# Kernel optimization log

Hardware: AMD Instinct MI355X
Metric: run time of the kernel (lower is better)

## Reference

```python
import jax, jax.numpy as jnp
import numpy as np


def setup_inputs() -> dict:
    key = jax.random.key(0)
    ks = jax.random.split(key, 7)
    B, C, N, D = 32, 256, 4096, 256
    s = 0.05
    return {
        "x": jax.random.normal(ks[0], (B, C, N), dtype=jnp.float32),
        "Wq": jax.random.normal(ks[1], (D, C), dtype=jnp.float32) * s,
        "bq": jax.random.normal(ks[2], (D,), dtype=jnp.float32) * s,
        "Wk": jax.random.normal(ks[3], (D, C), dtype=jnp.float32) * s,
        "bk": jax.random.normal(ks[4], (D,), dtype=jnp.float32) * s,
        "Wv": jax.random.normal(ks[5], (D, C), dtype=jnp.float32) * s,
        "bv": jax.random.normal(ks[6], (D,), dtype=jnp.float32) * s,
    }


def reference(x, Wq, bq, Wk, bk, Wv, bv):
    # 1x1 Conv1d == per-timestep linear: [B,C,N] x [D,C] -> [B,D,N]
    Q = jnp.einsum("bcn,dc->bdn", x, Wq) + bq[None, :, None]
    K = jnp.einsum("bcn,dc->bdn", x, Wk) + bk[None, :, None]
    V = jnp.einsum("bcn,dc->bdn", x, Wv) + bv[None, :, None]
    N = x.shape[-1]
    scale = 1.0 / jnp.sqrt(jnp.asarray(N, dtype=x.dtype))
    # channel-attention: scores are [B, D, D] (Q @ K^T over the time axis)
    scores = jnp.einsum("bdn,ben->bde", Q, K) * scale
    weights = jax.nn.softmax(scores, axis=-1)
    out = jnp.einsum("bde,ben->bdn", weights, V)  # [B, D, N]
    return out
```

## Files before the change

kernel.cpp:

```cpp
#include <hip/hip_runtime.h>
#include <cstdint>
#include <cstddef>


typedef float f32x4 __attribute__((ext_vector_type(4)));
typedef __bf16 bf16x8 __attribute__((ext_vector_type(8)));
typedef unsigned short u16;
typedef u16 u16x8 __attribute__((ext_vector_type(8)));
typedef u16 u16x4 __attribute__((ext_vector_type(4)));

__device__ __forceinline__ u16 f2bf(float f) {
    unsigned u = __builtin_bit_cast(unsigned, f);
    u += 0x7FFFu + ((u >> 16) & 1u);
    return (u16)(u >> 16);
}

__device__ __forceinline__ f32x4 mfma16(bf16x8 a, bf16x8 b, f32x4 c) {
    return __builtin_amdgcn_mfma_f32_16x16x32_bf16(a, b, c, 0, 0, 0);
}

__global__ void k_wvt(const float* __restrict__ Wv, u16* __restrict__ WvT) {
    const int eb = blockIdx.x;
    const int c  = threadIdx.x;
    u16x8 pk;
#pragma unroll
    for (int j = 0; j < 8; ++j) pk[j] = f2bf(Wv[(eb * 8 + j) * 256 + c]);
    *(u16x8*)&WvT[c * 256 + eb * 8] = pk;
}

__global__ void k_wcvt(const float* __restrict__ Wq, const float* __restrict__ Wk,
                       u16* __restrict__ Wqb, u16* __restrict__ Wkb) {
    const int m = blockIdx.x >> 5, chunk = blockIdx.x & 31;
    const float* src = m == 0 ? Wq : Wk;
    u16* dst = m == 0 ? Wqb : Wkb;
    const int i = chunk * 2048 + threadIdx.x * 8;
    f32x4 w0 = *(const f32x4*)(src + i);
    f32x4 w1 = *(const f32x4*)(src + i + 4);
    u16x8 pk;
    pk[0] = f2bf(w0[0]); pk[1] = f2bf(w0[1]); pk[2] = f2bf(w0[2]); pk[3] = f2bf(w0[3]);
    pk[4] = f2bf(w1[0]); pk[5] = f2bf(w1[1]); pk[6] = f2bf(w1[2]); pk[7] = f2bf(w1[3]);
    *(u16x8*)&dst[i] = pk;
}

__global__ __launch_bounds__(512, 2) void k_gram_p(const float* __restrict__ x,
                                                   float* __restrict__ Gpart,
                                                   float* __restrict__ rsum) {
    __shared__ __align__(16) u16 lds[2][256 * 64];
    __shared__ float ldsr[256];
    const int b = blockIdx.x >> 3, split = blockIdx.x & 7;
    const int t = threadIdx.x;
    const int lane = t & 63, wid = t >> 6;
    const int g = lane >> 4, q = lane & 15;

    if (t < 256) ldsr[t] = 0.f;

    f32x4 zero4 = {0.f, 0.f, 0.f, 0.f};
    f32x4 acc[2][16];
#pragma unroll
    for (int i = 0; i < 2; ++i)
#pragma unroll
        for (int j = 0; j < 16; ++j) acc[i][j] = zero4;

    const int c_st = t >> 1, half = t & 1;
    const int swz_w = (c_st & 7) << 3;
    const float* xp = x + ((size_t)b * 256 + c_st) * 4096 + split * 512 + half * 32;

    float s = 0.f;
    f32x4 R[8];
#pragma unroll
    for (int j = 0; j < 8; ++j) R[j] = *(const f32x4*)(xp + j * 4);
#pragma unroll
    for (int kk = 0; kk < 4; ++kk) {
        f32x4 w0 = R[2 * kk], w1 = R[2 * kk + 1];
        s += w0[0] + w0[1] + w0[2] + w0[3] + w1[0] + w1[1] + w1[2] + w1[3];
        u16x8 pk;
        pk[0] = f2bf(w0[0]); pk[1] = f2bf(w0[1]); pk[2] = f2bf(w0[2]); pk[3] = f2bf(w0[3]);
        pk[4] = f2bf(w1[0]); pk[5] = f2bf(w1[1]); pk[6] = f2bf(w1[2]); pk[7] = f2bf(w1[3]);
        *(u16x8*)&lds[0][(c_st * 64 + half * 32 + kk * 8) ^ swz_w] = pk;
    }
    __syncthreads();

    for (int nc = 0; nc < 8; ++nc) {
        const int cur = nc & 1;
        if (nc < 7) {
#pragma unroll
            for (int j = 0; j < 8; ++j) R[j] = *(const f32x4*)(xp + (nc + 1) * 64 + j * 4);
        }
#pragma unroll
        for (int ks = 0; ks < 2; ++ks) {
            const int c0 = 32 * wid + q;
            const int c1 = c0 + 16;
            bf16x8 a0 = *(const bf16x8*)&lds[cur][(c0 * 64 + ks * 32 + g * 8) ^ ((c0 & 7) << 3)];
            bf16x8 a1 = *(const bf16x8*)&lds[cur][(c1 * 64 + ks * 32 + g * 8) ^ ((c1 & 7) << 3)];
#pragma unroll
            for (int et = 0; et < 16; ++et) {
                const int c2 = et * 16 + q;
                bf16x8 bb = *(const bf16x8*)&lds[cur][(c2 * 64 + ks * 32 + g * 8) ^ ((c2 & 7) << 3)];
                acc[0][et] = mfma16(a0, bb, acc[0][et]);
                acc[1][et] = mfma16(a1, bb, acc[1][et]);
            }
        }
        if (nc < 7) {
#pragma unroll
            for (int kk = 0; kk < 4; ++kk) {
                f32x4 w0 = R[2 * kk], w1 = R[2 * kk + 1];
                s += w0[0] + w0[1] + w0[2] + w0[3] + w1[0] + w1[1] + w1[2] + w1[3];
                u16x8 pk;
                pk[0] = f2bf(w0[0]); pk[1] = f2bf(w0[1]); pk[2] = f2bf(w0[2]); pk[3] = f2bf(w0[3]);
                pk[4] = f2bf(w1[0]); pk[5] = f2bf(w1[1]); pk[6] = f2bf(w1[2]); pk[7] = f2bf(w1[3]);
                *(u16x8*)&lds[cur ^ 1][(c_st * 64 + half * 32 + kk * 8) ^ swz_w] = pk;
            }
        }
        __syncthreads();
    }

    atomicAdd(&ldsr[c_st], s);

    float* gp = Gpart + (size_t)(split * 32 + b) * 65536;
#pragma unroll
    for (int dt = 0; dt < 2; ++dt)
#pragma unroll
        for (int et = 0; et < 16; ++et)
#pragma unroll
            for (int rr = 0; rr < 4; ++rr) {
                const int cc = 32 * wid + dt * 16 + 4 * g + rr;
                const int c2 = et * 16 + q;
                gp[cc * 256 + c2] = acc[dt][et][rr];
            }
    __syncthreads();
    if (t < 256) atomicAdd(&rsum[b * 256 + t], ldsr[t]);
}

__global__ void k_reduce(const float* __restrict__ Gpart, u16* __restrict__ Gb) {
    const size_t j = (size_t)blockIdx.x * 2048 + threadIdx.x * 8;
    f32x4 s0 = {0.f, 0.f, 0.f, 0.f}, s1 = {0.f, 0.f, 0.f, 0.f};
#pragma unroll
    for (int s = 0; s < 8; ++s) {
        s0 += *(const f32x4*)(Gpart + (size_t)s * 2097152 + j);
        s1 += *(const f32x4*)(Gpart + (size_t)s * 2097152 + j + 4);
    }
    u16x8 pk;
    pk[0] = f2bf(s0[0]); pk[1] = f2bf(s0[1]); pk[2] = f2bf(s0[2]); pk[3] = f2bf(s0[3]);
    pk[4] = f2bf(s1[0]); pk[5] = f2bf(s1[1]); pk[6] = f2bf(s1[2]); pk[7] = f2bf(s1[3]);
    *(u16x8*)&Gb[j] = pk;
}

__global__ __launch_bounds__(512, 2) void k_gram(const float* __restrict__ x,
                                                 float* __restrict__ G,
                                                 float* __restrict__ rsum) {
    __shared__ __align__(16) u16 lds[256 * 64];
    __shared__ float ldsr[256];
    const int b = blockIdx.x >> 3, split = blockIdx.x & 7;
    const int t = threadIdx.x;
    const int lane = t & 63, wid = t >> 6;
    const int g = lane >> 4, q = lane & 15;

    if (t < 256) ldsr[t] = 0.f;

    f32x4 zero4 = {0.f, 0.f, 0.f, 0.f};
    f32x4 acc[2][16];
#pragma unroll
    for (int i = 0; i < 2; ++i)
#pragma unroll
        for (int j = 0; j < 16; ++j) acc[i][j] = zero4;

    const int c_st = t >> 1, half = t & 1;
    const int swz_w = (c_st & 7) << 3;
    const float* xp = x + ((size_t)b * 256 + c_st) * 4096 + split * 512 + half * 32;

    for (int nc = 0; nc < 8; ++nc) {
        __syncthreads();
        float s = 0.f;
#pragma unroll
        for (int kk = 0; kk < 4; ++kk) {
            f32x4 w0 = *(const f32x4*)(xp + nc * 64 + kk * 8);
            f32x4 w1 = *(const f32x4*)(xp + nc * 64 + kk * 8 + 4);
            s += w0[0] + w0[1] + w0[2] + w0[3] + w1[0] + w1[1] + w1[2] + w1[3];
            u16x8 pk;
            pk[0] = f2bf(w0[0]); pk[1] = f2bf(w0[1]); pk[2] = f2bf(w0[2]); pk[3] = f2bf(w0[3]);
            pk[4] = f2bf(w1[0]); pk[5] = f2bf(w1[1]); pk[6] = f2bf(w1[2]); pk[7] = f2bf(w1[3]);
            *(u16x8*)&lds[(c_st * 64 + half * 32 + kk * 8) ^ swz_w] = pk;
        }
        atomicAdd(&ldsr[c_st], s);
        __syncthreads();
#pragma unroll
        for (int ks = 0; ks < 2; ++ks) {
            const int c0 = 32 * wid + q;
            const int c1 = c0 + 16;
            bf16x8 a0 = *(const bf16x8*)&lds[(c0 * 64 + ks * 32 + g * 8) ^ ((c0 & 7) << 3)];
            bf16x8 a1 = *(const bf16x8*)&lds[(c1 * 64 + ks * 32 + g * 8) ^ ((c1 & 7) << 3)];
#pragma unroll
            for (int et = 0; et < 16; ++et) {
                const int c2 = et * 16 + q;
                bf16x8 bb = *(const bf16x8*)&lds[(c2 * 64 + ks * 32 + g * 8) ^ ((c2 & 7) << 3)];
                acc[0][et] = mfma16(a0, bb, acc[0][et]);
                acc[1][et] = mfma16(a1, bb, acc[1][et]);
            }
        }
    }
#pragma unroll
    for (int dt = 0; dt < 2; ++dt)
#pragma unroll
        for (int et = 0; et < 16; ++et)
#pragma unroll
            for (int rr = 0; rr < 4; ++rr) {
                const int cc = 32 * wid + dt * 16 + 4 * g + rr;
                const int c2 = et * 16 + q;
                atomicAdd(&G[((size_t)b * 256 + cc) * 256 + c2], acc[dt][et][rr]);
            }
    __syncthreads();
    if (t < 256) atomicAdd(&rsum[b * 256 + t], ldsr[t]);
}

__global__ void k_gcvt(const float* __restrict__ G, u16* __restrict__ Gb) {
    const size_t i = (size_t)blockIdx.x * 2048 + threadIdx.x * 8;
    f32x4 w0 = *(const f32x4*)(G + i);
    f32x4 w1 = *(const f32x4*)(G + i + 4);
    u16x8 pk;
    pk[0] = f2bf(w0[0]); pk[1] = f2bf(w0[1]); pk[2] = f2bf(w0[2]); pk[3] = f2bf(w0[3]);
    pk[4] = f2bf(w1[0]); pk[5] = f2bf(w1[1]); pk[6] = f2bf(w1[2]); pk[7] = f2bf(w1[3]);
    *(u16x8*)&Gb[i] = pk;
}

__global__ __launch_bounds__(512, 4) void k_T(const u16* __restrict__ Gb,
                                              const u16* __restrict__ Wkb,
                                              u16* __restrict__ Tws) {
    const int b = blockIdx.x >> 3, ebase = (blockIdx.x & 7) * 32;
    const int t = threadIdx.x;
    const int lane = t & 63, wid = t >> 6;
    const int g = lane >> 4, q = lane & 15;

    f32x4 zero4 = {0.f, 0.f, 0.f, 0.f};
    f32x4 acc[2][2];
#pragma unroll
    for (int i = 0; i < 2; ++i)
#pragma unroll
        for (int j = 0; j < 2; ++j) acc[i][j] = zero4;

    const u16* gp = Gb + (size_t)b * 65536;
#pragma unroll
    for (int ks = 0; ks < 8; ++ks) {
        bf16x8 a0 = *(const bf16x8*)&gp[(32 * wid + q) * 256 + ks * 32 + g * 8];
        bf16x8 a1 = *(const bf16x8*)&gp[(32 * wid + 16 + q) * 256 + ks * 32 + g * 8];
        bf16x8 b0 = *(const bf16x8*)&Wkb[(ebase + q) * 256 + ks * 32 + g * 8];
        bf16x8 b1 = *(const bf16x8*)&Wkb[(ebase + 16 + q) * 256 + ks * 32 + g * 8];
        acc[0][0] = mfma16(a0, b0, acc[0][0]);
        acc[0][1] = mfma16(a0, b1, acc[0][1]);
        acc[1][0] = mfma16(a1, b0, acc[1][0]);
        acc[1][1] = mfma16(a1, b1, acc[1][1]);
    }
#pragma unroll
    for (int dt = 0; dt < 2; ++dt)
#pragma unroll
        for (int etl = 0; etl < 2; ++etl) {
            const int e = ebase + etl * 16 + q;
            const int cb = 32 * wid + dt * 16 + 4 * g;
            u16x4 pk;
            pk[0] = f2bf(acc[dt][etl][0]); pk[1] = f2bf(acc[dt][etl][1]);
            pk[2] = f2bf(acc[dt][etl][2]); pk[3] = f2bf(acc[dt][etl][3]);
            *(u16x4*)&Tws[((size_t)b * 256 + e) * 256 + cb] = pk;
        }
}

__global__ __launch_bounds__(256, 2) void k_SWM(
    const u16* __restrict__ Tws, const float* __restrict__ rsum,
    const float* __restrict__ Wq, const u16* __restrict__ Wqb,
    const float* __restrict__ Wk,
    const float* __restrict__ bqv, const float* __restrict__ bkv,
    const float* __restrict__ bvv,
    const u16* __restrict__ WvT, u16* __restrict__ Mws, float* __restrict__ cpv) {
    __shared__ __align__(16) u16 Wlds[64 * 256];
    __shared__ float r_[256], v_[256], bk_[256], bv_[256], u_[64], bq_[64];
    const int b = blockIdx.x >> 2, dbase = (blockIdx.x & 3) * 64;
    const int t = threadIdx.x;
    const int lane = t & 63, wid = t >> 6;
    const int g = lane >> 4, q = lane & 15;

    r_[t] = rsum[b * 256 + t];
    bk_[t] = bkv[t];
    bv_[t] = bvv[t];
    if (t < 64) bq_[t] = bqv[dbase + t];
    __syncthreads();

    {
        float s = 0.f; const float* wp = Wk + (size_t)t * 256;
#pragma unroll 4
        for (int c = 0; c < 256; c += 4) {
            f32x4 w = *(const f32x4*)(wp + c);
            f32x4 rr = *(const f32x4*)(&r_[c]);
            s += w[0] * rr[0] + w[1] * rr[1] + w[2] * rr[2] + w[3] * rr[3];
        }
        v_[t] = s;
    }
    if (t < 64) {
        float s = 0.f; const float* wp = Wq + (size_t)(dbase + t) * 256;
#pragma unroll 4
        for (int c = 0; c < 256; c += 4) {
            f32x4 w = *(const f32x4*)(wp + c);
            f32x4 rr = *(const f32x4*)(&r_[c]);
            s += w[0] * rr[0] + w[1] * rr[1] + w[2] * rr[2] + w[3] * rr[3];
        }
        u_[t] = s;
    }
    __syncthreads();

    f32x4 zero4 = {0.f, 0.f, 0.f, 0.f};
    f32x4 acc[16];
#pragma unroll
    for (int j = 0; j < 16; ++j) acc[j] = zero4;

    const u16* tp = Tws + (size_t)b * 65536;
    const int d_l = wid * 16 + q;
#pragma unroll 2
    for (int ks = 0; ks < 8; ++ks) {
        bf16x8 bb = *(const bf16x8*)&Wqb[(dbase + d_l) * 256 + ks * 32 + g * 8];
#pragma unroll
        for (int et = 0; et < 16; ++et) {
            bf16x8 aa = *(const bf16x8*)&tp[(et * 16 + q) * 256 + ks * 32 + g * 8];
            acc[et] = mfma16(aa, bb, acc[et]);
        }
    }

    {
        const float ud = u_[d_l], bqd = bq_[d_l];
        float m = -3.4e38f;
#pragma unroll
        for (int et = 0; et < 16; ++et)
#pragma unroll
            for (int rr = 0; rr < 4; ++rr) {
                const int e = et * 16 + 4 * g + rr;
                float s = (acc[et][rr] + ud * bk_[e] + bqd * v_[e] + 4096.f * bqd * bk_[e]) * 0.015625f;
                acc[et][rr] = s;
                m = fmaxf(m, s);
            }
        m = fmaxf(m, __shfl_xor(m, 16));
        m = fmaxf(m, __shfl_xor(m, 32));
        float lsum = 0.f;
#pragma unroll
        for (int et = 0; et < 16; ++et)
#pragma unroll
            for (int rr = 0; rr < 4; ++rr) {
                float p = __expf(acc[et][rr] - m);
                acc[et][rr] = p;
                lsum += p;
            }
        lsum += __shfl_xor(lsum, 16);
        lsum += __shfl_xor(lsum, 32);
        const float inv = 1.f / lsum;
        float cp = 0.f;
#pragma unroll
        for (int et = 0; et < 16; ++et)
#pragma unroll
            for (int rr = 0; rr < 4; ++rr) {
                const int e = et * 16 + 4 * g + rr;
                float w = acc[et][rr] * inv;
                acc[et][rr] = w;
                cp += w * bv_[e];
            }
        cp += __shfl_xor(cp, 16);
        cp += __shfl_xor(cp, 32);
        if (g == 0) cpv[b * 256 + dbase + d_l] = cp;
    }

#pragma unroll
    for (int et = 0; et < 16; ++et) {
        u16x4 pk;
        pk[0] = f2bf(acc[et][0]); pk[1] = f2bf(acc[et][1]);
        pk[2] = f2bf(acc[et][2]); pk[3] = f2bf(acc[et][3]);
        *(u16x4*)&Wlds[(d_l * 256 + et * 16 + 4 * g) ^ ((d_l & 7) << 3)] = pk;
    }
    __syncthreads();

    f32x4 acc2[4][4];
#pragma unroll
    for (int i = 0; i < 4; ++i)
#pragma unroll
        for (int j = 0; j < 4; ++j) acc2[i][j] = zero4;

#pragma unroll 2
    for (int ks = 0; ks < 8; ++ks) {
        bf16x8 afr[4], bfr[4];
#pragma unroll
        for (int ct = 0; ct < 4; ++ct)
            afr[ct] = *(const bf16x8*)&WvT[(64 * wid + ct * 16 + q) * 256 + ks * 32 + g * 8];
#pragma unroll
        for (int j = 0; j < 4; ++j) {
            const int dl = j * 16 + q;
            bfr[j] = *(const bf16x8*)&Wlds[(dl * 256 + ks * 32 + g * 8) ^ ((dl & 7) << 3)];
        }
#pragma unroll
        for (int ct = 0; ct < 4; ++ct)
#pragma unroll
            for (int j = 0; j < 4; ++j)
                acc2[ct][j] = mfma16(afr[ct], bfr[j], acc2[ct][j]);
    }
#pragma unroll
    for (int ct = 0; ct < 4; ++ct)
#pragma unroll
        for (int j = 0; j < 4; ++j) {
            const int d = dbase + j * 16 + q;
            const int cb = 64 * wid + ct * 16 + 4 * g;
            u16x4 pk;
            pk[0] = f2bf(acc2[ct][j][0]); pk[1] = f2bf(acc2[ct][j][1]);
            pk[2] = f2bf(acc2[ct][j][2]); pk[3] = f2bf(acc2[ct][j][3]);
            *(u16x4*)&Mws[((size_t)b * 256 + d) * 256 + cb] = pk;
        }
}

__global__ __launch_bounds__(512, 2) void k_out(const float* __restrict__ x,
                                                const u16* __restrict__ Mws,
                                                const float* __restrict__ cpv,
                                                float* __restrict__ out) {
    __shared__ __align__(16) u16 xt[2][256 * 64];
    __shared__ float cp_l[256];
    const int b = blockIdx.x >> 4, nt = blockIdx.x & 15;
    const int n0 = nt * 256;
    const int t = threadIdx.x;
    const int lane = t & 63, wid = t >> 6;
    const int g = lane >> 4, q = lane & 15;

    if (t < 256) cp_l[t] = cpv[b * 256 + t];

    f32x4 zero4 = {0.f, 0.f, 0.f, 0.f};
    f32x4 acc[2][16];
#pragma unroll
    for (int i = 0; i < 2; ++i)
#pragma unroll
        for (int j = 0; j < 16; ++j) acc[i][j] = zero4;

    const int c8 = t & 7;
    const int n4 = t >> 3;
    const float* xbase = x + (size_t)b * 256 * 4096 + n0 + n4 * 4;
    const u16* mp = Mws + (size_t)b * 65536;

    f32x4 R[2][4];
#pragma unroll
    for (int sub = 0; sub < 2; ++sub) {
        const int cc0 = (c8 + 8 * sub) * 4;
#pragma unroll
        for (int j = 0; j < 4; ++j)
            R[sub][j] = *(const f32x4*)(xbase + (size_t)(cc0 + j) * 4096);
    }
#pragma unroll
    for (int sub = 0; sub < 2; ++sub)
#pragma unroll
        for (int j = 0; j < 4; ++j) {
            const int n = n4 * 4 + j;
            u16x4 pk;
            pk[0] = f2bf(R[sub][0][j]); pk[1] = f2bf(R[sub][1][j]);
            pk[2] = f2bf(R[sub][2][j]); pk[3] = f2bf(R[sub][3][j]);
            *(u16x4*)&xt[0][(n * 64 + (c8 + 8 * sub) * 4) ^ ((n & 7) << 3)] = pk;
        }
    __syncthreads();

    for (int ci = 0; ci < 4; ++ci) {
        const int cur = ci & 1;
        if (ci < 3) {
#pragma unroll
            for (int sub = 0; sub < 2; ++sub) {
                const int cc0 = (ci + 1) * 64 + (c8 + 8 * sub) * 4;
#pragma unroll
                for (int j = 0; j < 4; ++j)
                    R[sub][j] = *(const f32x4*)(xbase + (size_t)(cc0 + j) * 4096);
            }
        }
#pragma unroll
        for (int ks = 0; ks < 2; ++ks) {
            bf16x8 a0 = *(const bf16x8*)&mp[(32 * wid + q) * 256 + ci * 64 + ks * 32 + g * 8];
            bf16x8 a1 = *(const bf16x8*)&mp[(32 * wid + 16 + q) * 256 + ci * 64 + ks * 32 + g * 8];
#pragma unroll
            for (int ntl = 0; ntl < 16; ++ntl) {
                const int nn = ntl * 16 + q;
                bf16x8 bb = *(const bf16x8*)&xt[cur][(nn * 64 + ks * 32 + g * 8) ^ ((nn & 7) << 3)];
                acc[0][ntl] = mfma16(a0, bb, acc[0][ntl]);
                acc[1][ntl] = mfma16(a1, bb, acc[1][ntl]);
            }
        }
        if (ci < 3) {
#pragma unroll
            for (int sub = 0; sub < 2; ++sub)
#pragma unroll
                for (int j = 0; j < 4; ++j) {
                    const int n = n4 * 4 + j;
                    u16x4 pk;
                    pk[0] = f2bf(R[sub][0][j]); pk[1] = f2bf(R[sub][1][j]);
                    pk[2] = f2bf(R[sub][2][j]); pk[3] = f2bf(R[sub][3][j]);
                    *(u16x4*)&xt[cur ^ 1][(n * 64 + (c8 + 8 * sub) * 4) ^ ((n & 7) << 3)] = pk;
                }
        }
        __syncthreads();
    }

#pragma unroll
    for (int dt = 0; dt < 2; ++dt)
#pragma unroll
        for (int ntl = 0; ntl < 16; ++ntl)
#pragma unroll
            for (int rr = 0; rr < 4; ++rr) {
                const int d = 32 * wid + dt * 16 + 4 * g + rr;
                const int n = n0 + ntl * 16 + q;
                __builtin_nontemporal_store(acc[dt][ntl][rr] + cp_l[d],
                                            &out[((size_t)b * 256 + d) * 4096 + n]);
            }
}

extern "C" void kernel_launch(void* const* d_in, const int* in_sizes, int n_in,
                              void* d_out, int out_size, void* d_ws, size_t ws_size,
                              hipStream_t stream) {
    const float* x  = (const float*)d_in[0];
    const float* Wq = (const float*)d_in[1];
    const float* bq = (const float*)d_in[2];
    const float* Wk = (const float*)d_in[3];
    const float* bk = (const float*)d_in[4];
    const float* Wv = (const float*)d_in[5];
    const float* bv = (const float*)d_in[6];
    float* out = (float*)d_out;
    char* ws = (char*)d_ws;

    const size_t NEED_FAST = 71761920;

    if (ws_size >= NEED_FAST) {
        float* Gpart = (float*)(ws);
        u16*   Tws   = (u16*)  (ws);
        u16*   Mws   = (u16*)  (ws + 4194304);
        u16*   Gb    = (u16*)  (ws + 67108864);
        float* rsum  = (float*)(ws + 71303168);
        float* cpv   = (float*)(ws + 71335936);
        u16*   WvT   = (u16*)  (ws + 71368704);
        u16*   Wqb   = (u16*)  (ws + 71499776);
        u16*   Wkb   = (u16*)  (ws + 71630848);

        hipMemsetAsync(ws + 71303168, 0, 32768, stream);

        hipLaunchKernelGGL(k_wvt,    dim3(32),   dim3(256), 0, stream, Wv, WvT);
        hipLaunchKernelGGL(k_wcvt,   dim3(64),   dim3(256), 0, stream, Wq, Wk, Wqb, Wkb);
        hipLaunchKernelGGL(k_gram_p, dim3(256),  dim3(512), 0, stream, x, Gpart, rsum);
        hipLaunchKernelGGL(k_reduce, dim3(1024), dim3(256), 0, stream, Gpart, Gb);
        hipLaunchKernelGGL(k_T,      dim3(256),  dim3(512), 0, stream, Gb, Wkb, Tws);
        hipLaunchKernelGGL(k_SWM,    dim3(128),  dim3(256), 0, stream,
                           Tws, rsum, Wq, Wqb, Wk, bq, bk, bv, WvT, Mws, cpv);
        hipLaunchKernelGGL(k_out,    dim3(512),  dim3(512), 0, stream, x, Mws, cpv, out);
    } else {
        float* G    = (float*)(ws);
        u16*   Tws  = (u16*)  (ws);
        u16*   Gb   = (u16*)  (ws + 8388608);
        u16*   Mws  = (u16*)  (ws + 8388608);
        float* rsum = (float*)(ws + 12582912);
        float* cpv  = (float*)(ws + 12615680);
        u16*   WvT  = (u16*)  (ws + 12648448);
        u16*   Wqb  = (u16*)  (ws + 12779520);
        u16*   Wkb  = (u16*)  (ws + 12910592);

        hipMemsetAsync(ws, 0, 8388608, stream);
        hipMemsetAsync(ws + 12582912, 0, 32768, stream);

        hipLaunchKernelGGL(k_wvt,  dim3(32),   dim3(256), 0, stream, Wv, WvT);
        hipLaunchKernelGGL(k_wcvt, dim3(64),   dim3(256), 0, stream, Wq, Wk, Wqb, Wkb);
        hipLaunchKernelGGL(k_gram, dim3(256),  dim3(512), 0, stream, x, G, rsum);
        hipLaunchKernelGGL(k_gcvt, dim3(1024), dim3(256), 0, stream, G, Gb);
        hipLaunchKernelGGL(k_T,    dim3(256),  dim3(512), 0, stream, Gb, Wkb, Tws);
        hipLaunchKernelGGL(k_SWM,  dim3(128),  dim3(256), 0, stream,
                           Tws, rsum, Wq, Wqb, Wk, bq, bk, bv, WvT, Mws, cpv);
        hipLaunchKernelGGL(k_out,  dim3(512),  dim3(512), 0, stream, x, Mws, cpv, out);
    }
}
```

Measured before the change: 196.1 us.

## Precompute transposed bf16 x, store Gram partials in bf16, rewrite output GEMM

```diff
diff --git a/kernel.cpp b/kernel.cpp
--- a/kernel.cpp
+++ b/kernel.cpp
@@ -14,7 +14,10 @@
     u += 0x7FFFu + ((u >> 16) & 1u);
     return (u16)(u >> 16);
 }
-
+__device__ __forceinline__ float bf2f(u16 h) {
+    unsigned u = ((unsigned)h) << 16;
+    return __builtin_bit_cast(float, u);
+}
 __device__ __forceinline__ f32x4 mfma16(bf16x8 a, bf16x8 b, f32x4 c) {
     return __builtin_amdgcn_mfma_f32_16x16x32_bf16(a, b, c, 0, 0, 0);
 }
@@ -42,18 +45,58 @@
     *(u16x8*)&dst[i] = pk;
 }
 
-__global__ __launch_bounds__(512, 2) void k_gram_p(const float* __restrict__ x,
-                                                   float* __restrict__ Gpart,
-                                                   float* __restrict__ rsum) {
+__global__ __launch_bounds__(512, 2) void k_cvt(const float* __restrict__ x,
+                                                u16* __restrict__ xbt,
+                                                float* __restrict__ rsum) {
+    __shared__ float ldsr[256];
+    const int b = blockIdx.x >> 4, nchunk = blockIdx.x & 15;
+    const int nwin = nchunk * 256;
+    const int t = threadIdx.x;
+    const int cg = t & 63, ng = t >> 6;
+    const int c0 = cg * 4;
+
+    if (t < 256) ldsr[t] = 0.f;
+    __syncthreads();
+
+    const float* xp = x + ((size_t)b * 256 + c0) * 4096 + nwin + ng * 8;
+    u16* xtp = xbt + ((size_t)b * 4096 + nwin + ng * 8) * 256 + c0;
+
+    float rs[4] = {0.f, 0.f, 0.f, 0.f};
+#pragma unroll
+    for (int nc = 0; nc < 4; ++nc) {
+        f32x4 R[4][2];
+#pragma unroll
+        for (int i = 0; i < 4; ++i) {
+            R[i][0] = *(const f32x4*)(xp + (size_t)i * 4096 + nc * 64);
+            R[i][1] = *(const f32x4*)(xp + (size_t)i * 4096 + nc * 64 + 4);
+        }
+#pragma unroll
+        for (int i = 0; i < 4; ++i)
+#pragma unroll
+            for (int p = 0; p < 2; ++p)
+                rs[i] += R[i][p][0] + R[i][p][1] + R[i][p][2] + R[i][p][3];
+#pragma unroll
+        for (int j = 0; j < 8; ++j) {
+            u16x4 pk;
+#pragma unroll
+            for (int i = 0; i < 4; ++i) pk[i] = f2bf(R[i][j >> 2][j & 3]);
+            *(u16x4*)(xtp + (size_t)(nc * 64 + j) * 256) = pk;
+        }
+    }
+#pragma unroll
+    for (int i = 0; i < 4; ++i) atomicAdd(&ldsr[c0 + i], rs[i]);
+    __syncthreads();
+    if (t < 256) atomicAdd(&rsum[b * 256 + t], ldsr[t]);
+}
+
+__global__ __launch_bounds__(512, 2) void k_gram_l(const float* __restrict__ x,
+                                                   u16* __restrict__ Gpart) {
     __shared__ __align__(16) u16 lds[2][256 * 64];
-    __shared__ float ldsr[256];
     const int b = blockIdx.x >> 3, split = blockIdx.x & 7;
     const int t = threadIdx.x;
     const int lane = t & 63, wid = t >> 6;
     const int g = lane >> 4, q = lane & 15;
 
-    if (t < 256) ldsr[t] = 0.f;
-
     f32x4 zero4 = {0.f, 0.f, 0.f, 0.f};
     f32x4 acc[2][16];
 #pragma unroll
@@ -65,14 +108,12 @@
     const int swz_w = (c_st & 7) << 3;
     const float* xp = x + ((size_t)b * 256 + c_st) * 4096 + split * 512 + half * 32;
 
-    float s = 0.f;
     f32x4 R[8];
 #pragma unroll
     for (int j = 0; j < 8; ++j) R[j] = *(const f32x4*)(xp + j * 4);
 #pragma unroll
     for (int kk = 0; kk < 4; ++kk) {
         f32x4 w0 = R[2 * kk], w1 = R[2 * kk + 1];
-        s += w0[0] + w0[1] + w0[2] + w0[3] + w1[0] + w1[1] + w1[2] + w1[3];
         u16x8 pk;
         pk[0] = f2bf(w0[0]); pk[1] = f2bf(w0[1]); pk[2] = f2bf(w0[2]); pk[3] = f2bf(w0[3]);
         pk[4] = f2bf(w1[0]); pk[5] = f2bf(w1[1]); pk[6] = f2bf(w1[2]); pk[7] = f2bf(w1[3]);
@@ -104,7 +145,6 @@
 #pragma unroll
             for (int kk = 0; kk < 4; ++kk) {
                 f32x4 w0 = R[2 * kk], w1 = R[2 * kk + 1];
-                s += w0[0] + w0[1] + w0[2] + w0[3] + w1[0] + w1[1] + w1[2] + w1[3];
                 u16x8 pk;
                 pk[0] = f2bf(w0[0]); pk[1] = f2bf(w0[1]); pk[2] = f2bf(w0[2]); pk[3] = f2bf(w0[3]);
                 pk[4] = f2bf(w1[0]); pk[5] = f2bf(w1[1]); pk[6] = f2bf(w1[2]); pk[7] = f2bf(w1[3]);
@@ -114,9 +154,7 @@
         __syncthreads();
     }
 
-    atomicAdd(&ldsr[c_st], s);
-
-    float* gp = Gpart + (size_t)(split * 32 + b) * 65536;
+    u16* gp = Gpart + (size_t)(split * 32 + b) * 65536;
 #pragma unroll
     for (int dt = 0; dt < 2; ++dt)
 #pragma unroll
@@ -124,102 +162,25 @@
 #pragma unroll
             for (int rr = 0; rr < 4; ++rr) {
                 const int cc = 32 * wid + dt * 16 + 4 * g + rr;
-                const int c2 = et * 16 + q;
-                gp[cc * 256 + c2] = acc[dt][et][rr];
-            }
-    __syncthreads();
-    if (t < 256) atomicAdd(&rsum[b * 256 + t], ldsr[t]);
-}
-
-__global__ void k_reduce(const float* __restrict__ Gpart, u16* __restrict__ Gb) {
-    const size_t j = (size_t)blockIdx.x * 2048 + threadIdx.x * 8;
-    f32x4 s0 = {0.f, 0.f, 0.f, 0.f}, s1 = {0.f, 0.f, 0.f, 0.f};
-#pragma unroll
-    for (int s = 0; s < 8; ++s) {
-        s0 += *(const f32x4*)(Gpart + (size_t)s * 2097152 + j);
-        s1 += *(const f32x4*)(Gpart + (size_t)s * 2097152 + j + 4);
+                gp[cc * 256 + et * 16 + q] = f2bf(acc[dt][et][rr]);
+            }
+}
+
+__global__ void k_reduce_b(const u16* __restrict__ Gpart, u16* __restrict__ Gb) {
+    const size_t j = ((size_t)blockIdx.x * 256 + threadIdx.x) * 8;
+    float s[8];
+#pragma unroll
+    for (int i = 0; i < 8; ++i) s[i] = 0.f;
+#pragma unroll
+    for (int sp = 0; sp < 8; ++sp) {
+        u16x8 v = *(const u16x8*)(Gpart + (size_t)sp * 2097152 + j);
+#pragma unroll
+        for (int i = 0; i < 8; ++i) s[i] += bf2f(v[i]);
     }
     u16x8 pk;
-    pk[0] = f2bf(s0[0]); pk[1] = f2bf(s0[1]); pk[2] = f2bf(s0[2]); pk[3] = f2bf(s0[3]);
-    pk[4] = f2bf(s1[0]); pk[5] = f2bf(s1[1]); pk[6] = f2bf(s1[2]); pk[7] = f2bf(s1[3]);
+#pragma unroll
+    for (int i = 0; i < 8; ++i) pk[i] = f2bf(s[i]);
     *(u16x8*)&Gb[j] = pk;
-}
-
-__global__ __launch_bounds__(512, 2) void k_gram(const float* __restrict__ x,
-                                                 float* __restrict__ G,
-                                                 float* __restrict__ rsum) {
-    __shared__ __align__(16) u16 lds[256 * 64];
-    __shared__ float ldsr[256];
-    const int b = blockIdx.x >> 3, split = blockIdx.x & 7;
-    const int t = threadIdx.x;
-    const int lane = t & 63, wid = t >> 6;
-    const int g = lane >> 4, q = lane & 15;
-
-    if (t < 256) ldsr[t] = 0.f;
-
-    f32x4 zero4 = {0.f, 0.f, 0.f, 0.f};
-    f32x4 acc[2][16];
-#pragma unroll
-    for (int i = 0; i < 2; ++i)
-#pragma unroll
-        for (int j = 0; j < 16; ++j) acc[i][j] = zero4;
-
-    const int c_st = t >> 1, half = t & 1;
-    const int swz_w = (c_st & 7) << 3;
-    const float* xp = x + ((size_t)b * 256 + c_st) * 4096 + split * 512 + half * 32;
-
-    for (int nc = 0; nc < 8; ++nc) {
-        __syncthreads();
-        float s = 0.f;
-#pragma unroll
-        for (int kk = 0; kk < 4; ++kk) {
-            f32x4 w0 = *(const f32x4*)(xp + nc * 64 + kk * 8);
-            f32x4 w1 = *(const f32x4*)(xp + nc * 64 + kk * 8 + 4);
-            s += w0[0] + w0[1] + w0[2] + w0[3] + w1[0] + w1[1] + w1[2] + w1[3];
-            u16x8 pk;
-            pk[0] = f2bf(w0[0]); pk[1] = f2bf(w0[1]); pk[2] = f2bf(w0[2]); pk[3] = f2bf(w0[3]);
-            pk[4] = f2bf(w1[0]); pk[5] = f2bf(w1[1]); pk[6] = f2bf(w1[2]); pk[7] = f2bf(w1[3]);
-            *(u16x8*)&lds[(c_st * 64 + half * 32 + kk * 8) ^ swz_w] = pk;
-        }
-        atomicAdd(&ldsr[c_st], s);
-        __syncthreads();
-#pragma unroll
-        for (int ks = 0; ks < 2; ++ks) {
-            const int c0 = 32 * wid + q;
-            const int c1 = c0 + 16;
-            bf16x8 a0 = *(const bf16x8*)&lds[(c0 * 64 + ks * 32 + g * 8) ^ ((c0 & 7) << 3)];
-            bf16x8 a1 = *(const bf16x8*)&lds[(c1 * 64 + ks * 32 + g * 8) ^ ((c1 & 7) << 3)];
-#pragma unroll
-            for (int et = 0; et < 16; ++et) {
-                const int c2 = et * 16 + q;
-                bf16x8 bb = *(const bf16x8*)&lds[(c2 * 64 + ks * 32 + g * 8) ^ ((c2 & 7) << 3)];
-                acc[0][et] = mfma16(a0, bb, acc[0][et]);
-                acc[1][et] = mfma16(a1, bb, acc[1][et]);
-            }
-        }
-    }
-#pragma unroll
-    for (int dt = 0; dt < 2; ++dt)
-#pragma unroll
-        for (int et = 0; et < 16; ++et)
-#pragma unroll
-            for (int rr = 0; rr < 4; ++rr) {
-                const int cc = 32 * wid + dt * 16 + 4 * g + rr;
-                const int c2 = et * 16 + q;
-                atomicAdd(&G[((size_t)b * 256 + cc) * 256 + c2], acc[dt][et][rr]);
-            }
-    __syncthreads();
-    if (t < 256) atomicAdd(&rsum[b * 256 + t], ldsr[t]);
-}
-
-__global__ void k_gcvt(const float* __restrict__ G, u16* __restrict__ Gb) {
-    const size_t i = (size_t)blockIdx.x * 2048 + threadIdx.x * 8;
-    f32x4 w0 = *(const f32x4*)(G + i);
-    f32x4 w1 = *(const f32x4*)(G + i + 4);
-    u16x8 pk;
-    pk[0] = f2bf(w0[0]); pk[1] = f2bf(w0[1]); pk[2] = f2bf(w0[2]); pk[3] = f2bf(w0[3]);
-    pk[4] = f2bf(w1[0]); pk[5] = f2bf(w1[1]); pk[6] = f2bf(w1[2]); pk[7] = f2bf(w1[3]);
-    *(u16x8*)&Gb[i] = pk;
 }
 
 __global__ __launch_bounds__(512, 4) void k_T(const u16* __restrict__ Gb,
@@ -407,6 +368,156 @@
         }
 }
 
+__global__ __launch_bounds__(256, 4) void k_out_d(const u16* __restrict__ xbt,
+                                                  const u16* __restrict__ Mws,
+                                                  const float* __restrict__ cpv,
+                                                  float* __restrict__ out) {
+    const int b = blockIdx.x >> 6, nt = blockIdx.x & 63;
+    const int t = threadIdx.x;
+    const int lane = t & 63, w = t >> 6;
+    const int g = lane >> 4, q = lane & 15;
+
+    f32x4 zero4 = {0.f, 0.f, 0.f, 0.f};
+    f32x4 acc[4][4];
+#pragma unroll
+    for (int i = 0; i < 4; ++i)
+#pragma unroll
+        for (int j = 0; j < 4; ++j) acc[i][j] = zero4;
+
+    const u16* mp = Mws + (size_t)b * 65536 + (size_t)(w * 64 + q) * 256;
+    const u16* xp = xbt + ((size_t)b * 4096 + nt * 64 + q) * 256;
+
+#pragma unroll 2
+    for (int ks = 0; ks < 8; ++ks) {
+        const int ko = ks * 32 + g * 8;
+        bf16x8 A[4], B[4];
+#pragma unroll
+        for (int dt = 0; dt < 4; ++dt) A[dt] = *(const bf16x8*)&mp[(size_t)(dt * 16) * 256 + ko];
+#pragma unroll
+        for (int jt = 0; jt < 4; ++jt) B[jt] = *(const bf16x8*)&xp[(size_t)(jt * 16) * 256 + ko];
+#pragma unroll
+        for (int dt = 0; dt < 4; ++dt)
+#pragma unroll
+            for (int jt = 0; jt < 4; ++jt)
+                acc[dt][jt] = mfma16(A[dt], B[jt], acc[dt][jt]);
+    }
+
+#pragma unroll
+    for (int dt = 0; dt < 4; ++dt)
+#pragma unroll
+        for (int rr = 0; rr < 4; ++rr) {
+            const int d = w * 64 + dt * 16 + 4 * g + rr;
+            const float cp = cpv[b * 256 + d];
+            float* op = out + ((size_t)b * 256 + d) * 4096 + nt * 64 + q;
+#pragma unroll
+            for (int jt = 0; jt < 4; ++jt)
+                op[jt * 16] = acc[dt][jt][rr] + cp;
+        }
+}
+
+__global__ __launch_bounds__(512, 2) void k_gram_p(const float* __restrict__ x,
+                                                   float* __restrict__ Gpart,
+                                                   float* __restrict__ rsum) {
+    __shared__ __align__(16) u16 lds[2][256 * 64];
+    __shared__ float ldsr[256];
+    const int b = blockIdx.x >> 3, split = blockIdx.x & 7;
+    const int t = threadIdx.x;
+    const int lane = t & 63, wid = t >> 6;
+    const int g = lane >> 4, q = lane & 15;
+
+    if (t < 256) ldsr[t] = 0.f;
+
+    f32x4 zero4 = {0.f, 0.f, 0.f, 0.f};
+    f32x4 acc[2][16];
+#pragma unroll
+    for (int i = 0; i < 2; ++i)
+#pragma unroll
+        for (int j = 0; j < 16; ++j) acc[i][j] = zero4;
+
+    const int c_st = t >> 1, half = t & 1;
+    const int swz_w = (c_st & 7) << 3;
+    const float* xp = x + ((size_t)b * 256 + c_st) * 4096 + split * 512 + half * 32;
+
+    float s = 0.f;
+    f32x4 R[8];
+#pragma unroll
+    for (int j = 0; j < 8; ++j) R[j] = *(const f32x4*)(xp + j * 4);
+#pragma unroll
+    for (int kk = 0; kk < 4; ++kk) {
+        f32x4 w0 = R[2 * kk], w1 = R[2 * kk + 1];
+        s += w0[0] + w0[1] + w0[2] + w0[3] + w1[0] + w1[1] + w1[2] + w1[3];
+        u16x8 pk;
+        pk[0] = f2bf(w0[0]); pk[1] = f2bf(w0[1]); pk[2] = f2bf(w0[2]); pk[3] = f2bf(w0[3]);
+        pk[4] = f2bf(w1[0]); pk[5] = f2bf(w1[1]); pk[6] = f2bf(w1[2]); pk[7] = f2bf(w1[3]);
+        *(u16x8*)&lds[0][(c_st * 64 + half * 32 + kk * 8) ^ swz_w] = pk;
+    }
+    __syncthreads();
+
+    for (int nc = 0; nc < 8; ++nc) {
+        const int cur = nc & 1;
+        if (nc < 7) {
+#pragma unroll
+            for (int j = 0; j < 8; ++j) R[j] = *(const f32x4*)(xp + (nc + 1) * 64 + j * 4);
+        }
+#pragma unroll
+        for (int ks = 0; ks < 2; ++ks) {
+            const int c0 = 32 * wid + q;
+            const int c1 = c0 + 16;
+            bf16x8 a0 = *(const bf16x8*)&lds[cur][(c0 * 64 + ks * 32 + g * 8) ^ ((c0 & 7) << 3)];
+            bf16x8 a1 = *(const bf16x8*)&lds[cur][(c1 * 64 + ks * 32 + g * 8) ^ ((c1 & 7) << 3)];
+#pragma unroll
+            for (int et = 0; et < 16; ++et) {
+                const int c2 = et * 16 + q;
+                bf16x8 bb = *(const bf16x8*)&lds[cur][(c2 * 64 + ks * 32 + g * 8) ^ ((c2 & 7) << 3)];
+                acc[0][et] = mfma16(a0, bb, acc[0][et]);
+                acc[1][et] = mfma16(a1, bb, acc[1][et]);
+            }
+        }
+        if (nc < 7) {
+#pragma unroll
+            for (int kk = 0; kk < 4; ++kk) {
+                f32x4 w0 = R[2 * kk], w1 = R[2 * kk + 1];
+                s += w0[0] + w0[1] + w0[2] + w0[3] + w1[0] + w1[1] + w1[2] + w1[3];
+                u16x8 pk;
+                pk[0] = f2bf(w0[0]); pk[1] = f2bf(w0[1]); pk[2] = f2bf(w0[2]); pk[3] = f2bf(w0[3]);
+                pk[4] = f2bf(w1[0]); pk[5] = f2bf(w1[1]); pk[6] = f2bf(w1[2]); pk[7] = f2bf(w1[3]);
+                *(u16x8*)&lds[cur ^ 1][(c_st * 64 + half * 32 + kk * 8) ^ swz_w] = pk;
+            }
+        }
+        __syncthreads();
+    }
+
+    atomicAdd(&ldsr[c_st], s);
+
+    float* gp = Gpart + (size_t)(split * 32 + b) * 65536;
+#pragma unroll
+    for (int dt = 0; dt < 2; ++dt)
+#pragma unroll
+        for (int et = 0; et < 16; ++et)
+#pragma unroll
+            for (int rr = 0; rr < 4; ++rr) {
+                const int cc = 32 * wid + dt * 16 + 4 * g + rr;
+                const int c2 = et * 16 + q;
+                gp[cc * 256 + c2] = acc[dt][et][rr];
+            }
+    __syncthreads();
+    if (t < 256) atomicAdd(&rsum[b * 256 + t], ldsr[t]);
+}
+
+__global__ void k_reduce(const float* __restrict__ Gpart, u16* __restrict__ Gb) {
+    const size_t j = (size_t)blockIdx.x * 2048 + threadIdx.x * 8;
+    f32x4 s0 = {0.f, 0.f, 0.f, 0.f}, s1 = {0.f, 0.f, 0.f, 0.f};
+#pragma unroll
+    for (int s = 0; s < 8; ++s) {
+        s0 += *(const f32x4*)(Gpart + (size_t)s * 2097152 + j);
+        s1 += *(const f32x4*)(Gpart + (size_t)s * 2097152 + j + 4);
+    }
+    u16x8 pk;
+    pk[0] = f2bf(s0[0]); pk[1] = f2bf(s0[1]); pk[2] = f2bf(s0[2]); pk[3] = f2bf(s0[3]);
+    pk[4] = f2bf(s1[0]); pk[5] = f2bf(s1[1]); pk[6] = f2bf(s1[2]); pk[7] = f2bf(s1[3]);
+    *(u16x8*)&Gb[j] = pk;
+}
+
 __global__ __launch_bounds__(512, 2) void k_out(const float* __restrict__ x,
                                                 const u16* __restrict__ Mws,
                                                 const float* __restrict__ cpv,
@@ -499,8 +610,7 @@
             for (int rr = 0; rr < 4; ++rr) {
                 const int d = 32 * wid + dt * 16 + 4 * g + rr;
                 const int n = n0 + ntl * 16 + q;
-                __builtin_nontemporal_store(acc[dt][ntl][rr] + cp_l[d],
-                                            &out[((size_t)b * 256 + d) * 4096 + n]);
+                out[((size_t)b * 256 + d) * 4096 + n] = acc[dt][ntl][rr] + cp_l[d];
             }
 }
 
@@ -517,9 +627,33 @@
     float* out = (float*)d_out;
     char* ws = (char*)d_ws;
 
+    const size_t NEED_NEW  = 105316352;
     const size_t NEED_FAST = 71761920;
 
-    if (ws_size >= NEED_FAST) {
+    if (ws_size >= NEED_NEW) {
+        u16*   xbt   = (u16*)  (ws);
+        u16*   Gpart = (u16*)  (ws + 67108864);
+        u16*   Tws   = (u16*)  (ws + 67108864);
+        u16*   Mws   = (u16*)  (ws + 71303168);
+        u16*   Gb    = (u16*)  (ws + 100663296);
+        float* rsum  = (float*)(ws + 104857600);
+        float* cpv   = (float*)(ws + 104890368);
+        u16*   WvT   = (u16*)  (ws + 104923136);
+        u16*   Wqb   = (u16*)  (ws + 105054208);
+        u16*   Wkb   = (u16*)  (ws + 105185280);
+
+        hipMemsetAsync(ws + 104857600, 0, 32768, stream);
+
+        hipLaunchKernelGGL(k_wvt,      dim3(32),   dim3(256), 0, stream, Wv, WvT);
+        hipLaunchKernelGGL(k_wcvt,     dim3(64),   dim3(256), 0, stream, Wq, Wk, Wqb, Wkb);
+        hipLaunchKernelGGL(k_cvt,      dim3(512),  dim3(512), 0, stream, x, xbt, rsum);
+        hipLaunchKernelGGL(k_gram_l,   dim3(256),  dim3(512), 0, stream, x, Gpart);
+        hipLaunchKernelGGL(k_reduce_b, dim3(1024), dim3(256), 0, stream, Gpart, Gb);
+        hipLaunchKernelGGL(k_T,        dim3(256),  dim3(512), 0, stream, Gb, Wkb, Tws);
+        hipLaunchKernelGGL(k_SWM,      dim3(128),  dim3(256), 0, stream,
+                           Tws, rsum, Wq, Wqb, Wk, bq, bk, bv, WvT, Mws, cpv);
+        hipLaunchKernelGGL(k_out_d,    dim3(2048), dim3(256), 0, stream, xbt, Mws, cpv, out);
+    } else {
         float* Gpart = (float*)(ws);
         u16*   Tws   = (u16*)  (ws);
         u16*   Mws   = (u16*)  (ws + 4194304);
@@ -540,27 +674,5 @@
         hipLaunchKernelGGL(k_SWM,    dim3(128),  dim3(256), 0, stream,
                            Tws, rsum, Wq, Wqb, Wk, bq, bk, bv, WvT, Mws, cpv);
         hipLaunchKernelGGL(k_out,    dim3(512),  dim3(512), 0, stream, x, Mws, cpv, out);
-    } else {
-        float* G    = (float*)(ws);
-        u16*   Tws  = (u16*)  (ws);
-        u16*   Gb   = (u16*)  (ws + 8388608);
-        u16*   Mws  = (u16*)  (ws + 8388608);
-        float* rsum = (float*)(ws + 12582912);
-        float* cpv  = (float*)(ws + 12615680);
-        u16*   WvT  = (u16*)  (ws + 12648448);
-        u16*   Wqb  = (u16*)  (ws + 12779520);
-        u16*   Wkb  = (u16*)  (ws + 12910592);
-
-        hipMemsetAsync(ws, 0, 8388608, stream);
-        hipMemsetAsync(ws + 12582912, 0, 32768, stream);
-
-        hipLaunchKernelGGL(k_wvt,  dim3(32),   dim3(256), 0, stream, Wv, WvT);
-        hipLaunchKernelGGL(k_wcvt, dim3(64),   dim3(256), 0, stream, Wq, Wk, Wqb, Wkb);
-        hipLaunchKernelGGL(k_gram, dim3(256),  dim3(512), 0, stream, x, G, rsum);
-        hipLaunchKernelGGL(k_gcvt, dim3(1024), dim3(256), 0, stream, G, Gb);
-        hipLaunchKernelGGL(k_T,    dim3(256),  dim3(512), 0, stream, Gb, Wkb, Tws);
-        hipLaunchKernelGGL(k_SWM,  dim3(128),  dim3(256), 0, stream,
-                           Tws, rsum, Wq, Wqb, Wk, bq, bk, bv, WvT, Mws, cpv);
-        hipLaunchKernelGGL(k_out,  dim3(512),  dim3(512), 0, stream, x, Mws, cpv, out);
-    }
-}
+    }
+}
```

New measurement: 265.8 us. 1.36x slower.
